# Kernel optimization log

Measured on AMD Instinct MI355X. Metric: run time of the kernel, lower is better.

Reference implementation:

```python
import jax, jax.numpy as jnp
import numpy as np

TOP_K = 8
N_GROUP = 8
TOPK_GROUP = 4
ROUTED_SCALING = 2.5
NUM_EXPERTS = 256
HIDDEN = 4096
TOKENS = 16384


def setup_inputs() -> dict:
    key = jax.random.key(0)
    k1, k2 = jax.random.split(key)
    hidden_states = jax.random.normal(k1, (TOKENS, HIDDEN), dtype=jnp.float32)
    # Linear weight [num_experts, hidden]; scaled init for sane logits
    gate_w = jax.random.normal(k2, (NUM_EXPERTS, HIDDEN), dtype=jnp.float32) * (1.0 / np.sqrt(HIDDEN))
    expert_bias = jnp.zeros((NUM_EXPERTS,), dtype=jnp.float32)
    return {"hidden_states": hidden_states, "gate_w": gate_w, "expert_bias": expert_bias}


def _group_limited_topk(scores):
    # scores: [T, E]
    T, E = scores.shape
    g = scores.reshape(T, N_GROUP, E // N_GROUP)
    # sum of top-2 scores within each group -> group score [T, n_group]
    top2, _ = jax.lax.top_k(g, 2)
    group_scores = top2.sum(axis=-1)
    _, group_idx = jax.lax.top_k(group_scores, TOPK_GROUP)  # [T, topk_group]
    # group mask [T, n_group]
    group_mask = jax.nn.one_hot(group_idx, N_GROUP, dtype=scores.dtype).sum(axis=1) > 0
    score_mask = jnp.repeat(group_mask, E // N_GROUP, axis=1)  # [T, E]
    masked_scores = jnp.where(score_mask, scores, -jnp.inf)
    probs, top_indices = jax.lax.top_k(masked_scores, TOP_K)
    return probs, top_indices


def reference(hidden_states, gate_w, expert_bias):
    x = hidden_states.reshape(-1, hidden_states.shape[-1])
    logits = jnp.einsum("th,eh->te", x, gate_w).astype(jnp.float32)  # [T, E]
    scores = jax.nn.sigmoid(logits)
    scores_for_routing = scores + expert_bias[None, :]
    _, topk_idx = _group_limited_topk(scores_for_routing)  # [T, top_k]
    gathered = jnp.take_along_axis(scores, topk_idx, axis=1)  # [T, top_k]
    if TOP_K > 1:
        topk_weight = gathered / (gathered.sum(axis=-1, keepdims=True) + 1e-20)
    else:
        topk_weight = gathered
    topk_weight = topk_weight * ROUTED_SCALING
    return topk_idx, topk_weight, logits
```

## Files before the change

kernel.cpp:

```cpp
#include <hip/hip_runtime.h>
#include <math.h>

#define TOKENS  16384
#define HIDDEN  4096
#define NEXPERT 256
#define NGROUP  8
#define GSIZE   32
#define TOPKG   4
#define TOPK    8
#define RSCALE  2.5f

#define BM   64
#define BK   16
#define LDA  68
#define LDB  260
#define NTHR 512

__device__ __forceinline__ float sigmoid_acc(float x) {
    return 1.0f / (1.0f + expf(-x));
}

__global__ __launch_bounds__(NTHR, 2) __attribute__((amdgpu_waves_per_eu(2, 2)))
void moe_gate_fused(const float* __restrict__ A,
                    const float* __restrict__ B,
                    const float* __restrict__ bias,
                    float* __restrict__ out_idx,
                    float* __restrict__ out_w,
                    float* __restrict__ out_logits)
{
    __shared__ float As[2][BK * LDA];
    __shared__ float Bs[2][BK * LDB];
    __shared__ float gsum[BM][NGROUP + 1];

    const int tid = threadIdx.x;
    const int m0  = blockIdx.x * BM;

    const int ar_a = tid >> 3;
    const int kh   = tid & 7;
    const int ar_b = tid >> 1;
    const int q0   = (tid & 1) * 2;

    const float* Ag = A + (long)(m0 + ar_a) * HIDDEN + kh * 2;
    const float* Bg = B + (long)ar_b * HIDDEN + q0 * 4;

    const int tr   = tid >> 6;
    const int tc   = tid & 63;
    const int row0 = tr * 8;
    const int c0   = tc * 4;

    float2 qa;
    float4 pb0, pb1;

    qa  = *(const float2*)(Ag);
    pb0 = *(const float4*)(Bg);
    pb1 = *(const float4*)(Bg + 4);

    {
        float* as = As[0];
        as[(kh * 2 + 0) * LDA + ar_a] = qa.x;
        as[(kh * 2 + 1) * LDA + ar_a] = qa.y;
        float* bs = Bs[0];
        bs[(q0 * 4 + 0) * LDB + ar_b] = pb0.x;
        bs[(q0 * 4 + 1) * LDB + ar_b] = pb0.y;
        bs[(q0 * 4 + 2) * LDB + ar_b] = pb0.z;
        bs[(q0 * 4 + 3) * LDB + ar_b] = pb0.w;
        bs[(q0 * 4 + 4) * LDB + ar_b] = pb1.x;
        bs[(q0 * 4 + 5) * LDB + ar_b] = pb1.y;
        bs[(q0 * 4 + 6) * LDB + ar_b] = pb1.z;
        bs[(q0 * 4 + 7) * LDB + ar_b] = pb1.w;
    }
    __syncthreads();

    float acc[8][4] = {};

    const int NKT = HIDDEN / BK;
    for (int kt = 0; kt < NKT; ++kt) {
        const int cur = kt & 1;

        if (kt + 1 < NKT) {
            const int ko = (kt + 1) * BK;
            qa  = *(const float2*)(Ag + ko);
            pb0 = *(const float4*)(Bg + ko);
            pb1 = *(const float4*)(Bg + ko + 4);
        }

        const float* as = As[cur];
        const float* bs = Bs[cur];
        #pragma unroll
        for (int k = 0; k < BK; ++k) {
            float4 a0 = *(const float4*)(as + k * LDA + row0);
            float4 a1 = *(const float4*)(as + k * LDA + row0 + 4);
            float4 b0 = *(const float4*)(bs + k * LDB + c0);
            float av[8] = {a0.x, a0.y, a0.z, a0.w, a1.x, a1.y, a1.z, a1.w};
            float bv[4] = {b0.x, b0.y, b0.z, b0.w};
            #pragma unroll
            for (int i = 0; i < 8; ++i)
                #pragma unroll
                for (int j = 0; j < 4; ++j)
                    acc[i][j] = fmaf(av[i], bv[j], acc[i][j]);
        }

        if (kt + 1 < NKT) {
            float* as_w = As[cur ^ 1];
            as_w[(kh * 2 + 0) * LDA + ar_a] = qa.x;
            as_w[(kh * 2 + 1) * LDA + ar_a] = qa.y;
            float* bs_w = Bs[cur ^ 1];
            bs_w[(q0 * 4 + 0) * LDB + ar_b] = pb0.x;
            bs_w[(q0 * 4 + 1) * LDB + ar_b] = pb0.y;
            bs_w[(q0 * 4 + 2) * LDB + ar_b] = pb0.z;
            bs_w[(q0 * 4 + 3) * LDB + ar_b] = pb0.w;
            bs_w[(q0 * 4 + 4) * LDB + ar_b] = pb1.x;
            bs_w[(q0 * 4 + 5) * LDB + ar_b] = pb1.y;
            bs_w[(q0 * 4 + 6) * LDB + ar_b] = pb1.z;
            bs_w[(q0 * 4 + 7) * LDB + ar_b] = pb1.w;
        }
        __syncthreads();
    }

    #pragma unroll
    for (int i = 0; i < 8; ++i) {
        long row = m0 + row0 + i;
        *(float4*)(out_logits + row * NEXPERT + c0) =
            make_float4(acc[i][0], acc[i][1], acc[i][2], acc[i][3]);
    }
    __syncthreads();

    for (int task = tid; task < BM * NGROUP; task += NTHR) {
        const int tt = task >> 3;
        const int g  = task & 7;
        const float* lg = out_logits + (long)(m0 + tt) * NEXPERT + g * GSIZE;
        const float* bp = bias + g * GSIZE;
        float m1 = -INFINITY, m2 = -INFINITY;
        #pragma unroll
        for (int j4 = 0; j4 < GSIZE / 4; ++j4) {
            float4 l = *(const float4*)(lg + j4 * 4);
            float4 b = *(const float4*)(bp + j4 * 4);
            float vv[4] = {sigmoid_acc(l.x) + b.x, sigmoid_acc(l.y) + b.y,
                           sigmoid_acc(l.z) + b.z, sigmoid_acc(l.w) + b.w};
            #pragma unroll
            for (int c = 0; c < 4; ++c) {
                float x = vv[c];
                if (x > m1) { m2 = m1; m1 = x; }
                else if (x > m2) { m2 = x; }
            }
        }
        gsum[tt][g] = m1 + m2;
    }
    __syncthreads();

    if (tid < BM) {
        const long tok = m0 + tid;
        const float* lg = out_logits + tok * NEXPERT;

        float gs[NGROUP];
        #pragma unroll
        for (int g = 0; g < NGROUP; ++g) gs[g] = gsum[tid][g];

        unsigned selmask = 0;
        #pragma unroll
        for (int r = 0; r < TOPKG; ++r) {
            float best = -INFINITY; int bi = 0;
            #pragma unroll
            for (int g = 0; g < NGROUP; ++g) {
                bool taken = (selmask >> g) & 1u;
                if (!taken && gs[g] > best) { best = gs[g]; bi = g; }
            }
            selmask |= 1u << bi;
        }

        float rv[TOPK]; int ri[TOPK];
        #pragma unroll
        for (int k = 0; k < TOPK; ++k) { rv[k] = -INFINITY; ri[k] = 0; }

        for (int g = 0; g < NGROUP; ++g) {
            if (!((selmask >> g) & 1u)) continue;
            #pragma unroll 4
            for (int j = 0; j < GSIZE; ++j) {
                int e = g * GSIZE + j;
                float v = sigmoid_acc(lg[e]) + bias[e];
                if (v > rv[TOPK - 1]) {
                    rv[TOPK - 1] = v; ri[TOPK - 1] = e;
                    #pragma unroll
                    for (int q = TOPK - 1; q > 0; --q) {
                        if (rv[q] > rv[q - 1]) {
                            float tv = rv[q]; rv[q] = rv[q - 1]; rv[q - 1] = tv;
                            int   ti = ri[q]; ri[q] = ri[q - 1]; ri[q - 1] = ti;
                        }
                    }
                }
            }
        }

        float pv[TOPK]; float sum = 0.0f;
        #pragma unroll
        for (int k = 0; k < TOPK; ++k) { pv[k] = rv[k] - bias[ri[k]]; sum += pv[k]; }
        float denom = sum + 1e-20f;

        #pragma unroll
        for (int k = 0; k < TOPK; ++k) {
            out_idx[tok * TOPK + k] = (float)ri[k];
            out_w[tok * TOPK + k]   = pv[k] / denom * RSCALE;
        }
    }
}

extern "C" void kernel_launch(void* const* d_in, const int* in_sizes, int n_in,
                              void* d_out, int out_size, void* d_ws, size_t ws_size,
                              hipStream_t stream) {
    const float* hidden = (const float*)d_in[0];
    const float* gate_w = (const float*)d_in[1];
    const float* bias   = (const float*)d_in[2];

    float* out = (float*)d_out;
    float* out_idx    = out;
    float* out_w      = out + (long)TOKENS * TOPK;
    float* out_logits = out + (long)TOKENS * TOPK * 2;

    moe_gate_fused<<<TOKENS / BM, NTHR, 0, stream>>>(
        hidden, gate_w, bias, out_idx, out_w, out_logits);
}
```

Measured before the change: 742.5 us.

## Load A tile directly from global via wave-uniform scalar loads, drop A LDS staging

```diff
diff --git a/kernel.cpp b/kernel.cpp
--- a/kernel.cpp
+++ b/kernel.cpp
@@ -12,7 +12,6 @@
 
 #define BM   64
 #define BK   16
-#define LDA  68
 #define LDB  260
 #define NTHR 512
 
@@ -28,37 +27,28 @@
                     float* __restrict__ out_w,
                     float* __restrict__ out_logits)
 {
-    __shared__ float As[2][BK * LDA];
     __shared__ float Bs[2][BK * LDB];
     __shared__ float gsum[BM][NGROUP + 1];
 
     const int tid = threadIdx.x;
     const int m0  = blockIdx.x * BM;
 
-    const int ar_a = tid >> 3;
-    const int kh   = tid & 7;
     const int ar_b = tid >> 1;
     const int q0   = (tid & 1) * 2;
-
-    const float* Ag = A + (long)(m0 + ar_a) * HIDDEN + kh * 2;
     const float* Bg = B + (long)ar_b * HIDDEN + q0 * 4;
 
-    const int tr   = tid >> 6;
+    const int w8   = __builtin_amdgcn_readfirstlane(tid >> 6);
     const int tc   = tid & 63;
-    const int row0 = tr * 8;
+    const int row0 = w8 * 8;
     const int c0   = tc * 4;
 
-    float2 qa;
+    const float* Aw = A + (long)(m0 + row0) * HIDDEN;
+
     float4 pb0, pb1;
 
-    qa  = *(const float2*)(Ag);
     pb0 = *(const float4*)(Bg);
     pb1 = *(const float4*)(Bg + 4);
-
     {
-        float* as = As[0];
-        as[(kh * 2 + 0) * LDA + ar_a] = qa.x;
-        as[(kh * 2 + 1) * LDA + ar_a] = qa.y;
         float* bs = Bs[0];
         bs[(q0 * 4 + 0) * LDB + ar_b] = pb0.x;
         bs[(q0 * 4 + 1) * LDB + ar_b] = pb0.y;
@@ -79,31 +69,35 @@
 
         if (kt + 1 < NKT) {
             const int ko = (kt + 1) * BK;
-            qa  = *(const float2*)(Ag + ko);
             pb0 = *(const float4*)(Bg + ko);
             pb1 = *(const float4*)(Bg + ko + 4);
         }
 
-        const float* as = As[cur];
         const float* bs = Bs[cur];
-        #pragma unroll
-        for (int k = 0; k < BK; ++k) {
-            float4 a0 = *(const float4*)(as + k * LDA + row0);
-            float4 a1 = *(const float4*)(as + k * LDA + row0 + 4);
-            float4 b0 = *(const float4*)(bs + k * LDB + c0);
-            float av[8] = {a0.x, a0.y, a0.z, a0.w, a1.x, a1.y, a1.z, a1.w};
-            float bv[4] = {b0.x, b0.y, b0.z, b0.w};
+        const int kb = kt * BK;
+        #pragma unroll
+        for (int q = 0; q < 4; ++q) {
+            float4 aq[8];
             #pragma unroll
             for (int i = 0; i < 8; ++i)
+                aq[i] = *(const float4*)(Aw + i * HIDDEN + kb + q * 4);
+            #pragma unroll
+            for (int kk = 0; kk < 4; ++kk) {
+                const int k = q * 4 + kk;
+                float4 b0 = *(const float4*)(bs + k * LDB + c0);
                 #pragma unroll
-                for (int j = 0; j < 4; ++j)
-                    acc[i][j] = fmaf(av[i], bv[j], acc[i][j]);
+                for (int i = 0; i < 8; ++i) {
+                    float a = (kk == 0) ? aq[i].x : (kk == 1) ? aq[i].y
+                            : (kk == 2) ? aq[i].z : aq[i].w;
+                    acc[i][0] = fmaf(a, b0.x, acc[i][0]);
+                    acc[i][1] = fmaf(a, b0.y, acc[i][1]);
+                    acc[i][2] = fmaf(a, b0.z, acc[i][2]);
+                    acc[i][3] = fmaf(a, b0.w, acc[i][3]);
+                }
+            }
         }
 
         if (kt + 1 < NKT) {
-            float* as_w = As[cur ^ 1];
-            as_w[(kh * 2 + 0) * LDA + ar_a] = qa.x;
-            as_w[(kh * 2 + 1) * LDA + ar_a] = qa.y;
             float* bs_w = Bs[cur ^ 1];
             bs_w[(q0 * 4 + 0) * LDB + ar_b] = pb0.x;
             bs_w[(q0 * 4 + 1) * LDB + ar_b] = pb0.y;
```

Measured after the change: 993.6 us. 1.34x slower.
